# Optimization experiments

Hardware: AMD Instinct MI355X
Metric: run time of the kernel (lower is better)

Reference implementation:

```python
import jax, jax.numpy as jnp
import numpy as np

B, T, HIDDEN = 1, 2048, 2048
N_HEADS, N_KV_HEADS, HEAD_DIM = 32, 8, 64
N_KV_GROUPS = N_HEADS // N_KV_HEADS
MAX_POS = 8192


def _rope_tables(seq_len, head_dim, dtype):
    inv_freq = 1.0 / (10000.0 ** (jnp.arange(0, head_dim, 2, dtype=jnp.float32) / head_dim))
    t = jnp.arange(seq_len, dtype=jnp.float32)
    freqs = jnp.einsum('i,j->ij', t, inv_freq)          # [T, head_dim//2]
    emb = jnp.concatenate([freqs, freqs], axis=-1)      # [T, head_dim]
    cos = jnp.cos(emb)[None, None].astype(dtype)        # [1,1,T,head_dim]
    sin = jnp.sin(emb)[None, None].astype(dtype)
    return cos, sin


def _apply_rotary(x, cos, sin):
    # faithful to original: interleaved rotate-half with cat(freqs,freqs) tables
    x1, x2 = x[..., ::2], x[..., 1::2]
    x_rot = jnp.stack([-x2, x1], axis=-1).reshape(x.shape)
    return x * cos + x_rot * sin


def setup_inputs() -> dict:
    key = jax.random.key(0)
    kx, kq, kk, kv, ko = jax.random.split(key, 5)
    s = 0.02
    return {
        'x':  jax.random.normal(kx, (B, T, HIDDEN), dtype=jnp.float32),
        'Wq': s * jax.random.normal(kq, (N_HEADS * HEAD_DIM, HIDDEN), dtype=jnp.float32),
        'Wk': s * jax.random.normal(kk, (N_KV_HEADS * HEAD_DIM, HIDDEN), dtype=jnp.float32),
        'Wv': s * jax.random.normal(kv, (N_KV_HEADS * HEAD_DIM, HIDDEN), dtype=jnp.float32),
        'Wo': s * jax.random.normal(ko, (HIDDEN, HIDDEN), dtype=jnp.float32),
    }


def reference(x, Wq, Wk, Wv, Wo):
    Bv, Tv, _ = x.shape
    dtype = x.dtype
    # projections (torch Linear: y = x @ W.T), reshape to [B, heads, T, head_dim]
    q = jnp.einsum('bth,oh->bto', x, Wq).reshape(Bv, Tv, N_HEADS, HEAD_DIM).transpose(0, 2, 1, 3)
    k = jnp.einsum('bth,oh->bto', x, Wk).reshape(Bv, Tv, N_KV_HEADS, HEAD_DIM).transpose(0, 2, 1, 3)
    v = jnp.einsum('bth,oh->bto', x, Wv).reshape(Bv, Tv, N_KV_HEADS, HEAD_DIM).transpose(0, 2, 1, 3)
    cos, sin = _rope_tables(Tv, HEAD_DIM, dtype)
    q = _apply_rotary(q, cos, sin)
    k = _apply_rotary(k, cos, sin)
    if N_KV_GROUPS != 1:
        k = jnp.repeat(k, N_KV_GROUPS, axis=1)   # [B, n_heads, T, d]
        v = jnp.repeat(v, N_KV_GROUPS, axis=1)
    scale = 1.0 / jnp.sqrt(jnp.asarray(HEAD_DIM, dtype=dtype))
    scores = jnp.einsum('bhtd,bhsd->bhts', q, k) * scale   # [B,H,T,T]
    causal = jnp.tril(jnp.ones((Tv, Tv), dtype=bool))
    scores = jnp.where(causal[None, None], scores, jnp.asarray(-jnp.inf, dtype=dtype))
    attn = jax.nn.softmax(scores, axis=-1)
    out = jnp.einsum('bhts,bhsd->bhtd', attn, v)
    out = out.transpose(0, 2, 1, 3).reshape(Bv, Tv, HIDDEN)
    return jnp.einsum('bth,oh->bto', out, Wo)
```

## Files before the change

kernel.cpp:

```cpp
#include <hip/hip_runtime.h>
#include <hip/hip_bf16.h>
#include <stdint.h>

#define TT 2048
#define HID 2048
#define NH 32
#define NKV 8
#define HD 64

typedef __attribute__((ext_vector_type(4))) float f32x4;
typedef __attribute__((ext_vector_type(16))) float f32x16;
typedef __attribute__((ext_vector_type(8))) short bf16x8;

__device__ __forceinline__ unsigned short f2bf(float f) {
  unsigned int u = __builtin_bit_cast(unsigned int, f);
  unsigned int r = (u + 0x7FFFu + ((u >> 16) & 1u)) >> 16;
  return (unsigned short)r;
}
__device__ __forceinline__ float bf2f(unsigned short h) {
  unsigned int u = ((unsigned int)h) << 16;
  return __builtin_bit_cast(float, u);
}
__device__ __forceinline__ unsigned int cvtpk(float lo, float hi) {
  unsigned int d;
  asm("v_cvt_pk_bf16_f32 %0, %1, %2" : "=v"(d) : "v"(lo), "v"(hi));
  return d;
}

__device__ __forceinline__ void gld_lds16(const void* g, void* l) {
  __builtin_amdgcn_global_load_lds(
      (const __attribute__((address_space(1))) unsigned int*)g,
      (__attribute__((address_space(3))) unsigned int*)l,
      16, 0, 0);
}

__global__ __launch_bounds__(256)
void k_cvt_all(const float* __restrict__ x, const float* __restrict__ wq,
               const float* __restrict__ wk, const float* __restrict__ wv,
               const float* __restrict__ wo,
               unsigned short* __restrict__ xb, unsigned short* __restrict__ wqb,
               unsigned short* __restrict__ wkb, unsigned short* __restrict__ wvb,
               unsigned short* __restrict__ wob) {
  int i = blockIdx.x * 256 + threadIdx.x;
  const float* src; unsigned short* dst; int off;
  if      (i < 1048576) { src = x;  dst = xb;  off = i; }
  else if (i < 2097152) { src = wq; dst = wqb; off = i - 1048576; }
  else if (i < 2359296) { src = wk; dst = wkb; off = i - 2097152; }
  else if (i < 2621440) { src = wv; dst = wvb; off = i - 2359296; }
  else if (i < 3670016) { src = wo; dst = wob; off = i - 2621440; }
  else return;
  const float4 v = reinterpret_cast<const float4*>(src)[off];
  ushort4 o;
  o.x = f2bf(v.x); o.y = f2bf(v.y); o.z = f2bf(v.z); o.w = f2bf(v.w);
  reinterpret_cast<ushort4*>(dst)[off] = o;
}

__device__ __forceinline__ void stage_tile(const unsigned short* __restrict__ g,
                                           unsigned short* lds, int w, int l, int k0) {
#pragma unroll
  for (int j = 0; j < 2; ++j) {
    const int cbase = w * 128 + j * 64;
    const int c = cbase + l;
    const int row = c >> 2, off = c & 3;
    gld_lds16(g + row * 2048 + k0 + off * 8, lds + cbase * 8);
  }
}

__device__ __forceinline__ void gemm_core(const unsigned short* __restrict__ A,
                                          const unsigned short* __restrict__ B,
                                          unsigned short* As, unsigned short* Bs,
                                          f32x4 (&acc)[4][4], int kiters) {
  const int tid = threadIdx.x;
  const int l = tid & 63, w = tid >> 6;
  const int wm = w >> 1, wn = w & 1;
  const int ll = l & 15, lg = l >> 4;

  stage_tile(A, As, w, l, 0);
  stage_tile(B, Bs, w, l, 0);
  int cur = 0;
  for (int kt = 0; kt < kiters; ++kt) {
    __syncthreads();
    if (kt + 1 < kiters) {
      stage_tile(A, As + (cur ^ 1) * 4096, w, l, (kt + 1) * 32);
      stage_tile(B, Bs + (cur ^ 1) * 4096, w, l, (kt + 1) * 32);
    }
    const unsigned short* a0 = As + cur * 4096;
    const unsigned short* b0 = Bs + cur * 4096;
    bf16x8 af[4], bfr[4];
#pragma unroll
    for (int i = 0; i < 4; ++i) {
      af[i]  = *reinterpret_cast<const bf16x8*>(a0 + (wm * 64 + i * 16 + ll) * 32 + lg * 8);
      bfr[i] = *reinterpret_cast<const bf16x8*>(b0 + (wn * 64 + i * 16 + ll) * 32 + lg * 8);
    }
#pragma unroll
    for (int i = 0; i < 4; ++i)
#pragma unroll
      for (int j = 0; j < 4; ++j)
        acc[i][j] = __builtin_amdgcn_mfma_f32_16x16x32_bf16(af[i], bfr[j], acc[i][j], 0, 0, 0);
    cur ^= 1;
  }
}

__global__ __launch_bounds__(256)
void k_gemm_qkv(const unsigned short* __restrict__ xb,
                const unsigned short* __restrict__ wq,
                const unsigned short* __restrict__ wk,
                const unsigned short* __restrict__ wv,
                unsigned short* __restrict__ Pq,
                unsigned short* __restrict__ Pk,
                unsigned short* __restrict__ Pv) {
  __shared__ __align__(16) unsigned short As[2 * 4096];
  __shared__ __align__(16) unsigned short Bs[2 * 4096];
  const int bid = blockIdx.x;
  const unsigned short *A, *B;
  int m0, n0, seg, ks;
  if (bid < 640) {
    ks = bid & 1;
    int pair = bid >> 1;
    int mt = pair / 20, nt = pair % 20;
    m0 = mt * 128;
    A = xb + (size_t)m0 * 2048 + ks * 1024;
    if (nt < 16) { seg = 0; n0 = nt * 128; B = wq + (size_t)n0 * 2048 + ks * 1024; }
    else         { seg = 1; n0 = (nt - 16) * 128; B = wk + (size_t)n0 * 2048 + ks * 1024; }
  } else {
    int vb = bid - 640;
    ks = vb & 1;
    int pair = vb >> 1;
    int mt = pair / 16, nt = pair % 16;
    seg = 2; m0 = mt * 128; n0 = nt * 128;
    A = wv + (size_t)m0 * 2048 + ks * 1024;
    B = xb + (size_t)n0 * 2048 + ks * 1024;
  }
  f32x4 acc[4][4] = {};
  gemm_core(A, B, As, Bs, acc, 32);

  const int l = threadIdx.x & 63, w = threadIdx.x >> 6;
  const int wm = w >> 1, wn = w & 1;
#pragma unroll
  for (int i = 0; i < 4; ++i)
#pragma unroll
    for (int j = 0; j < 4; ++j)
#pragma unroll
      for (int r = 0; r < 4; ++r) {
        int row = m0 + wm * 64 + i * 16 + ((l >> 4) << 2) + r;
        int col = n0 + wn * 64 + j * 16 + (l & 15);
        unsigned short v = f2bf(acc[i][j][r]);
        if (seg == 0)      Pq[(size_t)ks * 4194304 + (size_t)row * 2048 + col] = v;
        else if (seg == 1) Pk[(size_t)ks * 1048576 + (size_t)row * 512 + col] = v;
        else               Pv[(size_t)ks * 1048576 + (size_t)row * 2048 + col] = v;
      }
}

__global__ __launch_bounds__(256)
void k_gemm_out(const unsigned short* __restrict__ Ob,
                const unsigned short* __restrict__ wo,
                float* __restrict__ out,
                unsigned short* __restrict__ P1,
                unsigned short* __restrict__ P2) {
  __shared__ __align__(16) unsigned short As[2 * 4096];
  __shared__ __align__(16) unsigned short Bs[2 * 4096];
  const int bid = blockIdx.x;
  const int ks = bid >> 8;
  const int rem = bid & 255;
  const int m0 = (rem >> 4) * 128, n0 = (rem & 15) * 128;
  const int k0 = (ks == 0) ? 0 : 704 + (ks - 1) * 672;
  const int kiters = (ks == 0) ? 22 : 21;
  f32x4 acc[4][4] = {};
  gemm_core(Ob + (size_t)m0 * 2048 + k0,
            wo + (size_t)n0 * 2048 + k0, As, Bs, acc, kiters);

  const int l = threadIdx.x & 63, w = threadIdx.x >> 6;
  const int wm = w >> 1, wn = w & 1;
#pragma unroll
  for (int i = 0; i < 4; ++i)
#pragma unroll
    for (int j = 0; j < 4; ++j)
#pragma unroll
      for (int r = 0; r < 4; ++r) {
        int row = m0 + wm * 64 + i * 16 + ((l >> 4) << 2) + r;
        int col = n0 + wn * 64 + j * 16 + (l & 15);
        if (ks == 0)      out[(size_t)row * HID + col] = acc[i][j][r];
        else if (ks == 1) P1[(size_t)row * HID + col] = f2bf(acc[i][j][r]);
        else              P2[(size_t)row * HID + col] = f2bf(acc[i][j][r]);
      }
}

__global__ __launch_bounds__(256)
void k_reduce_out(float* __restrict__ out,
                  const unsigned short* __restrict__ P1,
                  const unsigned short* __restrict__ P2) {
  const int i = blockIdx.x * 256 + threadIdx.x;
  float4 a = reinterpret_cast<const float4*>(out)[i];
  const ushort4 b = reinterpret_cast<const ushort4*>(P1)[i];
  const ushort4 c = reinterpret_cast<const ushort4*>(P2)[i];
  a.x += bf2f(b.x) + bf2f(c.x);
  a.y += bf2f(b.y) + bf2f(c.y);
  a.z += bf2f(b.z) + bf2f(c.z);
  a.w += bf2f(b.w) + bf2f(c.w);
  reinterpret_cast<float4*>(out)[i] = a;
}

__global__ __launch_bounds__(256)
void k_rope_tab(float2* __restrict__ tab) {
  const int i = blockIdx.x * 256 + threadIdx.x;
  const int t = i >> 6, k = i & 63;
  const float cexp = -13.287712379549449f / 32.0f;
  const float fr = exp2f((float)(k & 31) * cexp);
  const float a = (float)t * fr;
  tab[i] = make_float2(__cosf(a), __sinf(a));
}

__global__ __launch_bounds__(256)
void k_rope_apply(const unsigned short* __restrict__ Pk,
                  const unsigned short* __restrict__ Pv,
                  const unsigned short* __restrict__ Pq,
                  const float2* __restrict__ tab,
                  unsigned short* __restrict__ Kb,
                  unsigned short* __restrict__ VT,
                  unsigned short* __restrict__ Qb) {
  int p = blockIdx.x * 256 + threadIdx.x;
  if (p < 524288) {
    const int t = p >> 8;
    const int col2 = (p & 255) * 2;
    const int kh = col2 >> 6, d = col2 & 63;
    const unsigned int u0 = *reinterpret_cast<const unsigned int*>(Pk + (size_t)t * 512 + col2);
    const unsigned int u1 = *reinterpret_cast<const unsigned int*>(Pk + 1048576 + (size_t)t * 512 + col2);
    float x0 = bf2f((unsigned short)(u0 & 0xFFFFu)) + bf2f((unsigned short)(u1 & 0xFFFFu));
    float x1 = bf2f((unsigned short)(u0 >> 16)) + bf2f((unsigned short)(u1 >> 16));
    const float4 cs = *reinterpret_cast<const float4*>(tab + t * 64 + d);
    float o0 = x0 * cs.x - x1 * cs.y;
    float o1 = x1 * cs.z + x0 * cs.w;
    unsigned int pw = (unsigned int)f2bf(o0) | ((unsigned int)f2bf(o1) << 16);
    *reinterpret_cast<unsigned int*>(Kb + ((size_t)kh * 2048 + t) * 64 + d) = pw;
  } else if (p < 1048576) {
    const int i2 = (p - 524288) * 2;
    const unsigned int u0 = *reinterpret_cast<const unsigned int*>(Pv + i2);
    const unsigned int u1 = *reinterpret_cast<const unsigned int*>(Pv + 1048576 + i2);
    float x0 = bf2f((unsigned short)(u0 & 0xFFFFu)) + bf2f((unsigned short)(u1 & 0xFFFFu));
    float x1 = bf2f((unsigned short)(u0 >> 16)) + bf2f((unsigned short)(u1 >> 16));
    unsigned int pw = (unsigned int)f2bf(x0) | ((unsigned int)f2bf(x1) << 16);
    *reinterpret_cast<unsigned int*>(VT + i2) = pw;
  } else {
    const int pq = p - 1048576;
    const int t = pq >> 10;
    const int col2 = (pq & 1023) * 2;
    const int h = col2 >> 6, d = col2 & 63;
    const unsigned int u0 = *reinterpret_cast<const unsigned int*>(Pq + (size_t)t * 2048 + col2);
    const unsigned int u1 = *reinterpret_cast<const unsigned int*>(Pq + 4194304 + (size_t)t * 2048 + col2);
    float x0 = bf2f((unsigned short)(u0 & 0xFFFFu)) + bf2f((unsigned short)(u1 & 0xFFFFu));
    float x1 = bf2f((unsigned short)(u0 >> 16)) + bf2f((unsigned short)(u1 >> 16));
    const float scale = 0.125f * 1.4426950408889634f;
    const float4 cs = *reinterpret_cast<const float4*>(tab + t * 64 + d);
    float o0 = (x0 * cs.x - x1 * cs.y) * scale;
    float o1 = (x1 * cs.z + x0 * cs.w) * scale;
    unsigned int pw = (unsigned int)f2bf(o0) | ((unsigned int)f2bf(o1) << 16);
    *reinterpret_cast<unsigned int*>(Qb + ((size_t)h * 2048 + t) * 64 + d) = pw;
  }
}

__device__ __forceinline__ void attn_stage4(const unsigned short* __restrict__ Kg,
                                            const unsigned short* __restrict__ Vg,
                                            unsigned short* Ks, unsigned short* Vs,
                                            int kv0, int w, int l) {
#pragma unroll
  for (int j = 0; j < 2; ++j) {
    const int cb = j * 256 + w * 64;
    const int c = cb + l;
    const int row = c >> 3;
    const int src8 = ((c & 7) ^ (row & 7)) * 8;
    gld_lds16(Kg + (size_t)(kv0 + row) * 64 + src8, Ks + cb * 8);
    gld_lds16(Vg + (size_t)row * TT + kv0 + src8, Vs + cb * 8);
  }
}

__global__ __launch_bounds__(256, 2)
void k_attn(const unsigned short* __restrict__ Qb,
            const unsigned short* __restrict__ Kb,
            const unsigned short* __restrict__ VT,
            unsigned short* __restrict__ Ob) {
  __shared__ __align__(16) unsigned short S[17408];
  unsigned short* KsB = S;
  unsigned short* VsB = S + 8192;
  const int b = blockIdx.x;
  const int h = b & 31;
  const int i = b >> 5;
  const int p = (i < 8) ? (15 - i) : (i - 8);
  const int kh = h >> 2;
  const int tid = threadIdx.x;
  const int l = tid & 63, w = tid >> 6;
  const int q = l & 31, hi = l >> 5;
  const int qtw = 2 * p + (w >> 1);
  const int qrow = qtw * 64 + (w & 1) * 32 + q;
  const int nkt = 2 * p + 2;

  const unsigned short* Qh = Qb + (size_t)h * TT * 64;
  const unsigned short* Kh = Kb + (size_t)kh * TT * 64;
  const unsigned short* Vh = VT + (size_t)kh * 64 * TT;

  bf16x8 qf[4];
#pragma unroll
  for (int s = 0; s < 4; ++s)
    qf[s] = *reinterpret_cast<const bf16x8*>(Qh + (size_t)qrow * 64 + s * 16 + hi * 8);

  f32x16 ot0, ot1;
#pragma unroll
  for (int r = 0; r < 16; ++r) { ot0[r] = 0.f; ot1[r] = 0.f; }
  float lsum = 0.f;

  attn_stage4(Kh, Vh, KsB, VsB, 0, w, l);
  int cur = 0;
  for (int kt = 0; kt < nkt; ++kt) {
    __syncthreads();
    if (kt + 1 < nkt)
      attn_stage4(Kh, Vh, KsB + (cur ^ 1) * 4096, VsB + (cur ^ 1) * 4096,
                  (kt + 1) * 64, w, l);

    if (kt <= qtw) {
      const char* Kc = reinterpret_cast<const char*>(KsB + cur * 4096);
      const char* Vc = reinterpret_cast<const char*>(VsB + cur * 4096);

      f32x16 s0, s1;
#pragma unroll
      for (int r = 0; r < 16; ++r) { s0[r] = 0.f; s1[r] = 0.f; }
      __builtin_amdgcn_s_setprio(1);
#pragma unroll
      for (int s = 0; s < 4; ++s) {
        const int chunk = 2 * s + hi;
        const bf16x8 kf0 = *reinterpret_cast<const bf16x8*>(
            Kc + q * 128 + ((chunk ^ (q & 7)) * 16));
        const bf16x8 kf1 = *reinterpret_cast<const bf16x8*>(
            Kc + (32 + q) * 128 + ((chunk ^ (q & 7)) * 16));
        s0 = __builtin_amdgcn_mfma_f32_32x32x16_bf16(kf0, qf[s], s0, 0, 0, 0);
        s1 = __builtin_amdgcn_mfma_f32_32x32x16_bf16(kf1, qf[s], s1, 0, 0, 0);
      }
      __builtin_amdgcn_s_setprio(0);
      if (kt == qtw) {
#pragma unroll
        for (int r = 0; r < 16; ++r) {
          const int kvr = kt * 64 + (r & 3) + 8 * (r >> 2) + 4 * hi;
          if (kvr > qrow) s0[r] = -3e38f;
          if (kvr + 32 > qrow) s1[r] = -3e38f;
        }
      }
#pragma unroll
      for (int r = 0; r < 16; ++r) {
        s0[r] = __builtin_amdgcn_exp2f(s0[r] - 16.f);
        s1[r] = __builtin_amdgcn_exp2f(s1[r] - 16.f);
      }
      float t16[16];
#pragma unroll
      for (int r = 0; r < 16; ++r) t16[r] = s0[r] + s1[r];
#pragma unroll
      for (int r = 0; r < 8; ++r) t16[r] += t16[r + 8];
#pragma unroll
      for (int r = 0; r < 4; ++r) t16[r] += t16[r + 4];
      lsum += (t16[0] + t16[1]) + (t16[2] + t16[3]);

#pragma unroll
      for (int s = 0; s < 4; ++s) {
        const int base = (s & 1) * 8;
        const f32x16& sg = (s < 2) ? s0 : s1;
        const unsigned int c0 = cvtpk(sg[base + 0], sg[base + 1]);
        const unsigned int c1 = cvtpk(sg[base + 2], sg[base + 3]);
        const unsigned int c2 = cvtpk(sg[base + 4], sg[base + 5]);
        const unsigned int c3 = cvtpk(sg[base + 6], sg[base + 7]);
        const unsigned int slo = hi ? c0 : c2, shi_ = hi ? c1 : c3;
        const unsigned int rlo = (unsigned int)__shfl_xor((int)slo, 32);
        const unsigned int rhi = (unsigned int)__shfl_xor((int)shi_, 32);
        union { unsigned int u[4]; bf16x8 v; } P;
        P.u[0] = hi ? rlo : c0;
        P.u[1] = hi ? rhi : c1;
        P.u[2] = hi ? c2 : rlo;
        P.u[3] = hi ? c3 : rhi;
        const int chunk = 2 * s + hi;
        const bf16x8 vf0 = *reinterpret_cast<const bf16x8*>(
            Vc + q * 128 + ((chunk ^ (q & 7)) * 16));
        const bf16x8 vf1 = *reinterpret_cast<const bf16x8*>(
            Vc + (32 + q) * 128 + ((chunk ^ (q & 7)) * 16));
        __builtin_amdgcn_s_setprio(1);
        ot0 = __builtin_amdgcn_mfma_f32_32x32x16_bf16(vf0, P.v, ot0, 0, 0, 0);
        ot1 = __builtin_amdgcn_mfma_f32_32x32x16_bf16(vf1, P.v, ot1, 0, 0, 0);
        __builtin_amdgcn_s_setprio(0);
      }
    }
    cur ^= 1;
  }

  lsum += __shfl_xor(lsum, 32);
  __syncthreads();
  float* Of = reinterpret_cast<float*>(S) + w * (64 * 33);
  const float inv = 1.0f / lsum;
#pragma unroll
  for (int r = 0; r < 16; ++r) {
    const int d = (r & 3) + 8 * (r >> 2) + 4 * hi;
    Of[d * 33 + q] = ot0[r] * inv;
    Of[(d + 32) * 33 + q] = ot1[r] * inv;
  }
  __syncthreads();
#pragma unroll
  for (int i2 = 0; i2 < 4; ++i2) {
    const int a = 4 * hi + i2;
    float v[8];
#pragma unroll
    for (int k2 = 0; k2 < 8; ++k2) v[k2] = Of[(a * 8 + k2) * 33 + q];
    union { unsigned int u[4]; uint4 vec; } O4;
    O4.u[0] = cvtpk(v[0], v[1]);
    O4.u[1] = cvtpk(v[2], v[3]);
    O4.u[2] = cvtpk(v[4], v[5]);
    O4.u[3] = cvtpk(v[6], v[7]);
    *reinterpret_cast<uint4*>(Ob + (size_t)qrow * HID + h * 64 + a * 8) = O4.vec;
  }
}

extern "C" void kernel_launch(void* const* d_in, const int* in_sizes, int n_in,
                              void* d_out, int out_size, void* d_ws, size_t ws_size,
                              hipStream_t stream) {
  const float* x  = (const float*)d_in[0];
  const float* Wq = (const float*)d_in[1];
  const float* Wk = (const float*)d_in[2];
  const float* Wv = (const float*)d_in[3];
  const float* Wo = (const float*)d_in[4];
  float* out = (float*)d_out;
  char* ws = (char*)d_ws;

  unsigned short* xb  = (unsigned short*)(ws);
  unsigned short* wqb = (unsigned short*)(ws + (8u  << 20));
  unsigned short* wkb = (unsigned short*)(ws + (16u << 20));
  unsigned short* wvb = (unsigned short*)(ws + (18u << 20));
  unsigned short* wob = (unsigned short*)(ws + (20u << 20));
  unsigned short* Kb  = (unsigned short*)(ws + (36u << 20));
  unsigned short* VT  = (unsigned short*)(ws + (38u << 20));
  unsigned short* Ob  = xb;
  unsigned short* Qb  = (unsigned short*)(ws + (8u << 20));
  float2* tab = (float2*)(ws + (16u << 20));
  unsigned short* Pq = (unsigned short*)d_out;
  unsigned short* Pk = (unsigned short*)(ws + (28u << 20));
  unsigned short* Pv = (unsigned short*)(ws + (32u << 20));
  unsigned short* P1 = (unsigned short*)(ws + (28u << 20));
  unsigned short* P2 = (unsigned short*)(ws + (8u  << 20));

  k_cvt_all<<<14336, 256, 0, stream>>>(x, Wq, Wk, Wv, Wo, xb, wqb, wkb, wvb, wob);
  k_gemm_qkv<<<768, 256, 0, stream>>>(xb, wqb, wkb, wvb, Pq, Pk, Pv);
  k_rope_tab<<<512, 256, 0, stream>>>(tab);
  k_rope_apply<<<12288, 256, 0, stream>>>(Pk, Pv, Pq, tab, Kb, VT, Qb);
  k_attn<<<512, 256, 0, stream>>>(Qb, Kb, VT, Ob);
  k_gemm_out<<<768, 256, 0, stream>>>(Ob, wob, out, P1, P2);
  k_reduce_out<<<4096, 256, 0, stream>>>(out, P1, P2);
}
```

Before: 149.1 us.

## Stage GEMM epilogues through LDS for vector stores; fold rope table into convert

The QKV and output GEMM epilogues now write accumulators into a padded LDS tile, then each thread reads a contiguous 16-element row segment, packs it to bf16 (or keeps fp32), and writes it with 16-byte vector stores. This replaces scattered 2-byte and 4-byte global stores. Separately, the rope cos/sin table is computed by extra threads in the conversion kernel, which removes one kernel launch, and workspace offsets are reshuffled so the table does not collide. The cost is extra LDS traffic and barriers in the epilogue.

```diff
diff --git a/kernel.cpp b/kernel.cpp
--- a/kernel.cpp
+++ b/kernel.cpp
@@ -40,15 +40,24 @@
                const float* __restrict__ wo,
                unsigned short* __restrict__ xb, unsigned short* __restrict__ wqb,
                unsigned short* __restrict__ wkb, unsigned short* __restrict__ wvb,
-               unsigned short* __restrict__ wob) {
+               unsigned short* __restrict__ wob, float2* __restrict__ tab) {
   int i = blockIdx.x * 256 + threadIdx.x;
+  if (i >= 3670016) {
+    const int t2 = i - 3670016;
+    if (t2 >= 131072) return;
+    const int t = t2 >> 6, k = t2 & 63;
+    const float cexp = -13.287712379549449f / 32.0f;
+    const float fr = exp2f((float)(k & 31) * cexp);
+    const float a = (float)t * fr;
+    tab[t2] = make_float2(__cosf(a), __sinf(a));
+    return;
+  }
   const float* src; unsigned short* dst; int off;
   if      (i < 1048576) { src = x;  dst = xb;  off = i; }
   else if (i < 2097152) { src = wq; dst = wqb; off = i - 1048576; }
   else if (i < 2359296) { src = wk; dst = wkb; off = i - 2097152; }
   else if (i < 2621440) { src = wv; dst = wvb; off = i - 2359296; }
-  else if (i < 3670016) { src = wo; dst = wob; off = i - 2621440; }
-  else return;
+  else                  { src = wo; dst = wob; off = i - 2621440; }
   const float4 v = reinterpret_cast<const float4*>(src)[off];
   ushort4 o;
   o.x = f2bf(v.x); o.y = f2bf(v.y); o.z = f2bf(v.z); o.w = f2bf(v.w);
@@ -109,8 +118,7 @@
                 unsigned short* __restrict__ Pq,
                 unsigned short* __restrict__ Pk,
                 unsigned short* __restrict__ Pv) {
-  __shared__ __align__(16) unsigned short As[2 * 4096];
-  __shared__ __align__(16) unsigned short Bs[2 * 4096];
+  __shared__ __align__(16) unsigned short S[16384];
   const int bid = blockIdx.x;
   const unsigned short *A, *B;
   int m0, n0, seg, ks;
@@ -132,23 +140,40 @@
     B = xb + (size_t)n0 * 2048 + ks * 1024;
   }
   f32x4 acc[4][4] = {};
-  gemm_core(A, B, As, Bs, acc, 32);
-
-  const int l = threadIdx.x & 63, w = threadIdx.x >> 6;
-  const int wm = w >> 1, wn = w & 1;
-#pragma unroll
-  for (int i = 0; i < 4; ++i)
-#pragma unroll
-    for (int j = 0; j < 4; ++j)
-#pragma unroll
-      for (int r = 0; r < 4; ++r) {
-        int row = m0 + wm * 64 + i * 16 + ((l >> 4) << 2) + r;
-        int col = n0 + wn * 64 + j * 16 + (l & 15);
-        unsigned short v = f2bf(acc[i][j][r]);
-        if (seg == 0)      Pq[(size_t)ks * 4194304 + (size_t)row * 2048 + col] = v;
-        else if (seg == 1) Pk[(size_t)ks * 1048576 + (size_t)row * 512 + col] = v;
-        else               Pv[(size_t)ks * 1048576 + (size_t)row * 2048 + col] = v;
-      }
+  gemm_core(A, B, S, S + 8192, acc, 32);
+
+  unsigned short* dst0;
+  int rstride;
+  if (seg == 0)      { dst0 = Pq + (size_t)ks * 4194304; rstride = 2048; }
+  else if (seg == 1) { dst0 = Pk + (size_t)ks * 1048576; rstride = 512; }
+  else               { dst0 = Pv + (size_t)ks * 1048576; rstride = 2048; }
+  const int tid = threadIdx.x;
+  const int l = tid & 63, w = tid >> 6;
+  const int wm = w >> 1, wn = w & 1, ll = l & 15, lg = l >> 4;
+  float* T = reinterpret_cast<float*>(S);
+  const int lrow = tid >> 3, c = tid & 7;
+  const int grow0 = m0 + (lrow & 15) + (lrow >> 4) * 64;
+#pragma unroll
+  for (int i = 0; i < 4; ++i) {
+    __syncthreads();
+#pragma unroll
+    for (int j = 0; j < 4; ++j) {
+      const int lr0 = wm * 16 + lg * 4;
+      const int lc = wn * 64 + j * 16 + ll;
+#pragma unroll
+      for (int r = 0; r < 4; ++r) T[(lr0 + r) * 132 + lc] = acc[i][j][r];
+    }
+    __syncthreads();
+    const float* src = T + lrow * 132 + c * 16;
+    union { unsigned int u[4]; uint4 v; } A0, A1;
+#pragma unroll
+    for (int k2 = 0; k2 < 4; ++k2) A0.u[k2] = cvtpk(src[2 * k2], src[2 * k2 + 1]);
+#pragma unroll
+    for (int k2 = 0; k2 < 4; ++k2) A1.u[k2] = cvtpk(src[8 + 2 * k2], src[9 + 2 * k2]);
+    unsigned short* dst = dst0 + (size_t)(grow0 + i * 16) * rstride + n0 + c * 16;
+    *reinterpret_cast<uint4*>(dst) = A0.v;
+    *reinterpret_cast<uint4*>(dst + 8) = A1.v;
+  }
 }
 
 __global__ __launch_bounds__(256)
@@ -157,8 +182,7 @@
                 float* __restrict__ out,
                 unsigned short* __restrict__ P1,
                 unsigned short* __restrict__ P2) {
-  __shared__ __align__(16) unsigned short As[2 * 4096];
-  __shared__ __align__(16) unsigned short Bs[2 * 4096];
+  __shared__ __align__(16) unsigned short S[16384];
   const int bid = blockIdx.x;
   const int ks = bid >> 8;
   const int rem = bid & 255;
@@ -167,22 +191,44 @@
   const int kiters = (ks == 0) ? 22 : 21;
   f32x4 acc[4][4] = {};
   gemm_core(Ob + (size_t)m0 * 2048 + k0,
-            wo + (size_t)n0 * 2048 + k0, As, Bs, acc, kiters);
-
-  const int l = threadIdx.x & 63, w = threadIdx.x >> 6;
-  const int wm = w >> 1, wn = w & 1;
-#pragma unroll
-  for (int i = 0; i < 4; ++i)
-#pragma unroll
-    for (int j = 0; j < 4; ++j)
-#pragma unroll
-      for (int r = 0; r < 4; ++r) {
-        int row = m0 + wm * 64 + i * 16 + ((l >> 4) << 2) + r;
-        int col = n0 + wn * 64 + j * 16 + (l & 15);
-        if (ks == 0)      out[(size_t)row * HID + col] = acc[i][j][r];
-        else if (ks == 1) P1[(size_t)row * HID + col] = f2bf(acc[i][j][r]);
-        else              P2[(size_t)row * HID + col] = f2bf(acc[i][j][r]);
-      }
+            wo + (size_t)n0 * 2048 + k0, S, S + 8192, acc, kiters);
+
+  const int tid = threadIdx.x;
+  const int l = tid & 63, w = tid >> 6;
+  const int wm = w >> 1, wn = w & 1, ll = l & 15, lg = l >> 4;
+  float* T = reinterpret_cast<float*>(S);
+  const int lrow = tid >> 3, c = tid & 7;
+  const int grow0 = m0 + (lrow & 15) + (lrow >> 4) * 64;
+#pragma unroll
+  for (int i = 0; i < 4; ++i) {
+    __syncthreads();
+#pragma unroll
+    for (int j = 0; j < 4; ++j) {
+      const int lr0 = wm * 16 + lg * 4;
+      const int lc = wn * 64 + j * 16 + ll;
+#pragma unroll
+      for (int r = 0; r < 4; ++r) T[(lr0 + r) * 132 + lc] = acc[i][j][r];
+    }
+    __syncthreads();
+    const float* src = T + lrow * 132 + c * 16;
+    const int grow = grow0 + i * 16;
+    const int gcol = n0 + c * 16;
+    if (ks == 0) {
+      float* dst = out + (size_t)grow * HID + gcol;
+#pragma unroll
+      for (int k2 = 0; k2 < 4; ++k2)
+        reinterpret_cast<float4*>(dst)[k2] = *reinterpret_cast<const float4*>(src + 4 * k2);
+    } else {
+      union { unsigned int u[4]; uint4 v; } A0, A1;
+#pragma unroll
+      for (int k2 = 0; k2 < 4; ++k2) A0.u[k2] = cvtpk(src[2 * k2], src[2 * k2 + 1]);
+#pragma unroll
+      for (int k2 = 0; k2 < 4; ++k2) A1.u[k2] = cvtpk(src[8 + 2 * k2], src[9 + 2 * k2]);
+      unsigned short* dst = ((ks == 1) ? P1 : P2) + (size_t)grow * HID + gcol;
+      *reinterpret_cast<uint4*>(dst) = A0.v;
+      *reinterpret_cast<uint4*>(dst + 8) = A1.v;
+    }
+  }
 }
 
 __global__ __launch_bounds__(256)
@@ -198,16 +244,6 @@
   a.z += bf2f(b.z) + bf2f(c.z);
   a.w += bf2f(b.w) + bf2f(c.w);
   reinterpret_cast<float4*>(out)[i] = a;
-}
-
-__global__ __launch_bounds__(256)
-void k_rope_tab(float2* __restrict__ tab) {
-  const int i = blockIdx.x * 256 + threadIdx.x;
-  const int t = i >> 6, k = i & 63;
-  const float cexp = -13.287712379549449f / 32.0f;
-  const float fr = exp2f((float)(k & 31) * cexp);
-  const float a = (float)t * fr;
-  tab[i] = make_float2(__cosf(a), __sinf(a));
 }
 
 __global__ __launch_bounds__(256)
@@ -428,20 +464,19 @@
   unsigned short* wkb = (unsigned short*)(ws + (16u << 20));
   unsigned short* wvb = (unsigned short*)(ws + (18u << 20));
   unsigned short* wob = (unsigned short*)(ws + (20u << 20));
-  unsigned short* Kb  = (unsigned short*)(ws + (36u << 20));
+  unsigned short* Kb  = (unsigned short*)(ws + (18u << 20));
   unsigned short* VT  = (unsigned short*)(ws + (38u << 20));
   unsigned short* Ob  = xb;
   unsigned short* Qb  = (unsigned short*)(ws + (8u << 20));
-  float2* tab = (float2*)(ws + (16u << 20));
+  float2* tab = (float2*)(ws + (36u << 20));
   unsigned short* Pq = (unsigned short*)d_out;
   unsigned short* Pk = (unsigned short*)(ws + (28u << 20));
   unsigned short* Pv = (unsigned short*)(ws + (32u << 20));
   unsigned short* P1 = (unsigned short*)(ws + (28u << 20));
   unsigned short* P2 = (unsigned short*)(ws + (8u  << 20));
 
-  k_cvt_all<<<14336, 256, 0, stream>>>(x, Wq, Wk, Wv, Wo, xb, wqb, wkb, wvb, wob);
+  k_cvt_all<<<14848, 256, 0, stream>>>(x, Wq, Wk, Wv, Wo, xb, wqb, wkb, wvb, wob, tab);
   k_gemm_qkv<<<768, 256, 0, stream>>>(xb, wqb, wkb, wvb, Pq, Pk, Pv);
-  k_rope_tab<<<512, 256, 0, stream>>>(tab);
   k_rope_apply<<<12288, 256, 0, stream>>>(Pk, Pv, Pq, tab, Kb, VT, Qb);
   k_attn<<<512, 256, 0, stream>>>(Qb, Kb, VT, Ob);
   k_gemm_out<<<768, 256, 0, stream>>>(Ob, wob, out, P1, P2);
```

New measurement: 145.8 us. -2.2%, faster.
